# Optimization experiments

Measured on AMD Instinct MI355X. Metric: run time of the kernel, lower is better.

Reference implementation:

```python
import jax, jax.numpy as jnp
import numpy as np
import math

B, S, H, D = 4, 1024, 12, 64   # batch, max_seqlen, heads, head_dim
DIM = H * D                    # 768
L = 512                        # actual per-sequence length (unpadded)
NNZ = B * L                    # total non-pad tokens


def setup_inputs() -> dict:
    key = jax.random.key(0)
    k1, k2, k3 = jax.random.split(key, 3)
    hidden_states = jax.random.normal(k1, (NNZ, DIM), dtype=jnp.float32)
    Wqkv_w = jax.random.normal(k2, (3 * DIM, DIM), dtype=jnp.float32) * 0.02
    Wqkv_b = jnp.zeros((3 * DIM,), dtype=jnp.float32)
    # attn mask: first L tokens of each sequence are real
    attn_mask = (jnp.arange(S)[None, :] < L).astype(jnp.int32) * jnp.ones((B, 1), jnp.int32)
    # additive bias (e.g. ALiBi/relative-pos style) + key-padding penalty
    bias = jax.random.normal(k3, (B, H, S, S), dtype=jnp.float32) * 0.02
    bias = bias + jnp.where(attn_mask[:, None, None, :] == 1, 0.0, -10000.0)
    # flattened positions of non-pad tokens in the padded (B*S,) layout
    indices = (jnp.arange(B)[:, None] * S + jnp.arange(L)[None, :]).reshape(-1).astype(jnp.int64)
    cu_seqlens = (jnp.arange(B + 1) * L).astype(jnp.int32)
    return {
        "hidden_states": hidden_states,
        "Wqkv_w": Wqkv_w,
        "Wqkv_b": Wqkv_b,
        "bias": bias,
        "cu_seqlens": cu_seqlens,
        "max_seqlen_in_batch": S,
        "indices": indices,
        "attn_mask": attn_mask,
    }


def reference(hidden_states, Wqkv_w, Wqkv_b, bias, cu_seqlens, max_seqlen_in_batch, indices, attn_mask):
    b = cu_seqlens.shape[0] - 1
    s = max_seqlen_in_batch
    # QKV projection on unpadded tokens: (nnz, 3*dim)
    qkv = hidden_states @ Wqkv_w.T + Wqkv_b
    # pad_input: scatter tokens into padded (b*s, 3*dim) buffer
    padded = jnp.zeros((b * s, 3 * DIM), dtype=qkv.dtype).at[indices].set(qkv)
    qkv = padded.reshape(b, s, 3, H, D)
    q = qkv[:, :, 0]  # (b, s, h, d)
    k = qkv[:, :, 1]
    v = qkv[:, :, 2]
    scores = jnp.einsum("bqhd,bkhd->bhqk", q, k) / math.sqrt(D) + bias
    probs = jax.nn.softmax(scores, axis=-1)  # dropout p=0 -> identity
    attn = jnp.einsum("bhqk,bkhd->bqhd", probs, v)  # (b, s, h, d)
    # unpad_input_only: gather non-pad rows, flatten heads
    out = attn.reshape(b * s, H * D)[indices]  # (nnz, dim)
    return out
```

## Files before the change

### kernel.cpp

```cpp
#include <hip/hip_runtime.h>
#include <hip/hip_bf16.h>


typedef __attribute__((ext_vector_type(8))) __bf16 bf16x8;
typedef __attribute__((ext_vector_type(4))) __bf16 bf16x4;
typedef __attribute__((ext_vector_type(4))) float  f32x4;

static __device__ __forceinline__ __bf16 tobf(float x) { return (__bf16)x; }

__global__ __launch_bounds__(256) void cvt_bf16(const float* __restrict__ hid,
                                                const float* __restrict__ W,
                                                __bf16* __restrict__ hidB,
                                                __bf16* __restrict__ WB)
{
    int i = blockIdx.x * 256 + threadIdx.x;
    const float* src; __bf16* dst; int off;
    if (i < 196608) { src = hid; dst = hidB; off = i * 8; }
    else            { src = W;   dst = WB;   off = (i - 196608) * 8; }
    float4 a = *reinterpret_cast<const float4*>(src + off);
    float4 b = *reinterpret_cast<const float4*>(src + off + 4);
    bf16x8 o = { tobf(a.x), tobf(a.y), tobf(a.z), tobf(a.w),
                 tobf(b.x), tobf(b.y), tobf(b.z), tobf(b.w) };
    *reinterpret_cast<bf16x8*>(dst + off) = o;
}

__global__ __launch_bounds__(256) void qkv_gemm(
    const __bf16* __restrict__ hidB,
    const __bf16* __restrict__ WB,
    const float*  __restrict__ qb,
    __bf16* __restrict__ Qb, __bf16* __restrict__ Kb, __bf16* __restrict__ Vt)
{
    __shared__ char lds[24 * 1024];

    const int tid = threadIdx.x, lane = tid & 63, wave = tid >> 6;
    const int lo = lane & 15, hi = lane >> 4;
    const int wr = wave >> 1, wc = wave & 1;

    int flat = blockIdx.y * 36 + blockIdx.x;
    flat = (flat & 7) * 72 + (flat >> 3);
    const int f0 = (flat % 36) * 64;
    const int r0 = (flat / 36) * 128;

    const int srow  = tid >> 3;
    const int koffB = (tid & 7) * 16;
    const int kel   = (tid & 7) * 8;

    bf16x8 st[6];
#pragma unroll
    for (int p = 0; p < 4; ++p)
        st[p] = *reinterpret_cast<const bf16x8*>(hidB + (size_t)(r0 + p * 32 + srow) * 768 + kel);
#pragma unroll
    for (int p = 0; p < 2; ++p)
        st[4 + p] = *reinterpret_cast<const bf16x8*>(WB + (size_t)(f0 + p * 32 + srow) * 768 + kel);

    f32x4 acc[4][2] = {};

    for (int kt = 0; kt < 12; ++kt) {
        __syncthreads();
#pragma unroll
        for (int p = 0; p < 4; ++p) {
            int row = p * 32 + srow;
            *reinterpret_cast<bf16x8*>(lds + row * 128 + (koffB ^ ((row & 7) << 4))) = st[p];
        }
#pragma unroll
        for (int p = 0; p < 2; ++p) {
            int row = p * 32 + srow;
            *reinterpret_cast<bf16x8*>(lds + 16384 + row * 128 + (koffB ^ ((row & 7) << 4))) = st[4 + p];
        }
        if (kt < 11) {
            int k0 = (kt + 1) * 64 + kel;
#pragma unroll
            for (int p = 0; p < 4; ++p)
                st[p] = *reinterpret_cast<const bf16x8*>(hidB + (size_t)(r0 + p * 32 + srow) * 768 + k0);
#pragma unroll
            for (int p = 0; p < 2; ++p)
                st[4 + p] = *reinterpret_cast<const bf16x8*>(WB + (size_t)(f0 + p * 32 + srow) * 768 + k0);
        }
        __syncthreads();
#pragma unroll
        for (int ks = 0; ks < 2; ++ks) {
            bf16x8 bfrag[2];
#pragma unroll
            for (int fn = 0; fn < 2; ++fn) {
                int row = wc * 32 + fn * 16 + lo;
                bfrag[fn] = *reinterpret_cast<const bf16x8*>(
                    lds + 16384 + row * 128 + ((ks * 64 + hi * 16) ^ ((row & 7) << 4)));
            }
#pragma unroll
            for (int fm = 0; fm < 4; ++fm) {
                int row = wr * 64 + fm * 16 + lo;
                bf16x8 afrag = *reinterpret_cast<const bf16x8*>(
                    lds + row * 128 + ((ks * 64 + hi * 16) ^ ((row & 7) << 4)));
                acc[fm][0] = __builtin_amdgcn_mfma_f32_16x16x32_bf16(afrag, bfrag[0], acc[fm][0], 0, 0, 0);
                acc[fm][1] = __builtin_amdgcn_mfma_f32_16x16x32_bf16(afrag, bfrag[1], acc[fm][1], 0, 0, 0);
            }
        }
    }

#pragma unroll
    for (int fn = 0; fn < 2; ++fn) {
        int m = f0 + wc * 32 + fn * 16 + lo;
        float bv = qb[m];
        int sel = m / 768;
        int mm  = m - sel * 768;
        int hh  = mm >> 6, d = mm & 63;
        float scale = (sel == 0) ? 0.125f : 1.0f;
#pragma unroll
        for (int fm = 0; fm < 4; ++fm) {
            int t0 = r0 + wr * 64 + fm * 16 + hi * 4;
            int b  = t0 >> 9, q = t0 & 511;
            int bh = b * 12 + hh;
            float v[4];
#pragma unroll
            for (int j = 0; j < 4; ++j) v[j] = (acc[fm][fn][j] + bv) * scale;
            if (sel == 2) {
                bf16x4 pv = { tobf(v[0]), tobf(v[1]), tobf(v[2]), tobf(v[3]) };
                *reinterpret_cast<bf16x4*>(&Vt[((size_t)bh * 64 + d) * 512 + q]) = pv;
            } else {
                __bf16* dst = (sel == 0) ? Qb : Kb;
#pragma unroll
                for (int j = 0; j < 4; ++j)
                    dst[((size_t)bh * 512 + q + j) * 64 + d] = tobf(v[j]);
            }
        }
    }
}

__global__ __launch_bounds__(256) void attn_kernel(
    const __bf16* __restrict__ Qb, const __bf16* __restrict__ Kb,
    const __bf16* __restrict__ Vt, const float* __restrict__ bias,
    float* __restrict__ out)
{
    __shared__ __bf16 P[4][16][40];
    __shared__ float  Obuf[2][16][68];
    __shared__ float  Lbuf[2][16];

    const int tid = threadIdx.x, lane = tid & 63, wave = tid >> 6;
    const int lo = lane & 15, hi = lane >> 4;
    const int qt = wave >> 1, kp = wave & 1;
    const int bh = blockIdx.y, b = bh / 12, hd = bh % 12;
    const int q0 = blockIdx.x * 32 + qt * 16;

    const __bf16* Qp = Qb + ((size_t)bh * 512 + q0) * 64;
    bf16x8 qf0 = *reinterpret_cast<const bf16x8*>(Qp + lo * 64 + hi * 8);
    bf16x8 qf1 = *reinterpret_cast<const bf16x8*>(Qp + lo * 64 + 32 + hi * 8);

    const __bf16* Kbh = Kb + (size_t)bh * 512 * 64;
    const __bf16* Vbh = Vt + (size_t)bh * 64 * 512;
    const float*  bp  = bias + ((size_t)bh * 1024 + q0) * 1024;

    f32x4 oacc[4] = {};
    float lsum[4] = {0.f, 0.f, 0.f, 0.f};
    __bf16* Pw = &P[wave][0][0];

    for (int kc = 0; kc < 8; ++kc) {
        const int k0 = kp * 256 + kc * 32;
        f32x4 c0, c1;
#pragma unroll
        for (int j = 0; j < 4; ++j) {
            const float* r = bp + (size_t)(hi * 4 + j) * 1024 + k0;
            c0[j] = r[lo];
            c1[j] = r[16 + lo];
        }
        const __bf16* kr = Kbh + (size_t)(k0 + lo) * 64 + hi * 8;
        bf16x8 kf00 = *reinterpret_cast<const bf16x8*>(kr);
        bf16x8 kf01 = *reinterpret_cast<const bf16x8*>(kr + 32);
        bf16x8 kf10 = *reinterpret_cast<const bf16x8*>(kr + 16 * 64);
        bf16x8 kf11 = *reinterpret_cast<const bf16x8*>(kr + 16 * 64 + 32);
        f32x4 s0 = __builtin_amdgcn_mfma_f32_16x16x32_bf16(qf0, kf00, c0, 0, 0, 0);
        s0       = __builtin_amdgcn_mfma_f32_16x16x32_bf16(qf1, kf01, s0, 0, 0, 0);
        f32x4 s1 = __builtin_amdgcn_mfma_f32_16x16x32_bf16(qf0, kf10, c1, 0, 0, 0);
        s1       = __builtin_amdgcn_mfma_f32_16x16x32_bf16(qf1, kf11, s1, 0, 0, 0);

#pragma unroll
        for (int j = 0; j < 4; ++j) {
            float p0 = __expf(s0[j]), p1 = __expf(s1[j]);
            lsum[j] += p0 + p1;
            Pw[(hi * 4 + j) * 40 + lo]      = tobf(p0);
            Pw[(hi * 4 + j) * 40 + 16 + lo] = tobf(p1);
        }
        bf16x8 pf = *reinterpret_cast<const bf16x8*>(Pw + lo * 40 + hi * 8);
#pragma unroll
        for (int dt = 0; dt < 4; ++dt) {
            bf16x8 vf = *reinterpret_cast<const bf16x8*>(
                Vbh + (size_t)(dt * 16 + lo) * 512 + k0 + hi * 8);
            oacc[dt] = __builtin_amdgcn_mfma_f32_16x16x32_bf16(pf, vf, oacc[dt], 0, 0, 0);
        }
    }

#pragma unroll
    for (int j = 0; j < 4; ++j) {
        float s = lsum[j];
        s += __shfl_xor(s, 1, 64); s += __shfl_xor(s, 2, 64);
        s += __shfl_xor(s, 4, 64); s += __shfl_xor(s, 8, 64);
        lsum[j] = s;
    }

    if (kp == 1) {
#pragma unroll
        for (int dt = 0; dt < 4; ++dt)
#pragma unroll
            for (int j = 0; j < 4; ++j)
                Obuf[qt][hi * 4 + j][dt * 16 + lo] = oacc[dt][j];
        if (lo == 0) {
#pragma unroll
            for (int j = 0; j < 4; ++j) Lbuf[qt][hi * 4 + j] = lsum[j];
        }
    }
    __syncthreads();
    if (kp == 0) {
#pragma unroll
        for (int j = 0; j < 4; ++j) {
            float inv = 1.0f / (lsum[j] + Lbuf[qt][hi * 4 + j]);
            int q = q0 + hi * 4 + j;
            float* op = out + (size_t)(b * 512 + q) * 768 + hd * 64;
#pragma unroll
            for (int dt = 0; dt < 4; ++dt)
                op[dt * 16 + lo] = (oacc[dt][j] + Obuf[qt][hi * 4 + j][dt * 16 + lo]) * inv;
        }
    }
}

extern "C" void kernel_launch(void* const* d_in, const int* in_sizes, int n_in,
                              void* d_out, int out_size, void* d_ws, size_t ws_size,
                              hipStream_t stream) {
    const float* hid  = (const float*)d_in[0];
    const float* W    = (const float*)d_in[1];
    const float* qb   = (const float*)d_in[2];
    const float* bias = (const float*)d_in[3];
    float* out = (float*)d_out;

    char* ws = (char*)d_ws;
    __bf16* hidB = (__bf16*)(ws);
    __bf16* WB   = (__bf16*)(ws + 3145728);
    __bf16* Qb   = (__bf16*)(ws + 6684672);
    __bf16* Kb   = (__bf16*)(ws + 9830400);
    __bf16* Vt   = (__bf16*)(ws + 12976128);

    cvt_bf16<<<1632, 256, 0, stream>>>(hid, W, hidB, WB);
    qkv_gemm<<<dim3(36, 16), 256, 0, stream>>>(hidB, WB, qb, Qb, Kb, Vt);
    attn_kernel<<<dim3(16, 48), 256, 0, stream>>>(Qb, Kb, Vt, bias, out);
}
```

Before: 297.0 us.

## Fuse fp32-to-bf16 conversion into GEMM, double-buffer LDS, prefetch attention operands

Removes the separate conversion kernel: the QKV GEMM now loads fp32 inputs directly and converts them to bf16 while writing to a double-buffered LDS tile. This cuts one launch and a full round trip of the converted tensors through memory, and replaces two barriers per k-step with one. The attention kernel now prefetches the next chunk's bias, K and V fragments into registers, raises wave priority around the MFMAs, and swizzles the block order across a 1D grid. Together these raise register pressure and double the GEMM's LDS use, which may lower occupancy.

```diff
diff --git a/kernel.cpp b/kernel.cpp
--- a/kernel.cpp
+++ b/kernel.cpp
@@ -8,75 +8,65 @@
 
 static __device__ __forceinline__ __bf16 tobf(float x) { return (__bf16)x; }
 
-__global__ __launch_bounds__(256) void cvt_bf16(const float* __restrict__ hid,
-                                                const float* __restrict__ W,
-                                                __bf16* __restrict__ hidB,
-                                                __bf16* __restrict__ WB)
-{
-    int i = blockIdx.x * 256 + threadIdx.x;
-    const float* src; __bf16* dst; int off;
-    if (i < 196608) { src = hid; dst = hidB; off = i * 8; }
-    else            { src = W;   dst = WB;   off = (i - 196608) * 8; }
-    float4 a = *reinterpret_cast<const float4*>(src + off);
-    float4 b = *reinterpret_cast<const float4*>(src + off + 4);
-    bf16x8 o = { tobf(a.x), tobf(a.y), tobf(a.z), tobf(a.w),
-                 tobf(b.x), tobf(b.y), tobf(b.z), tobf(b.w) };
-    *reinterpret_cast<bf16x8*>(dst + off) = o;
-}
-
 __global__ __launch_bounds__(256) void qkv_gemm(
-    const __bf16* __restrict__ hidB,
-    const __bf16* __restrict__ WB,
-    const float*  __restrict__ qb,
+    const float* __restrict__ hid,
+    const float* __restrict__ W,
+    const float* __restrict__ qb,
     __bf16* __restrict__ Qb, __bf16* __restrict__ Kb, __bf16* __restrict__ Vt)
 {
-    __shared__ char lds[24 * 1024];
+    __shared__ char lds[2][24 * 1024];
 
     const int tid = threadIdx.x, lane = tid & 63, wave = tid >> 6;
     const int lo = lane & 15, hi = lane >> 4;
     const int wr = wave >> 1, wc = wave & 1;
 
-    int flat = blockIdx.y * 36 + blockIdx.x;
+    int flat = blockIdx.x;
     flat = (flat & 7) * 72 + (flat >> 3);
     const int f0 = (flat % 36) * 64;
     const int r0 = (flat / 36) * 128;
 
-    const int srow  = tid >> 3;
-    const int koffB = (tid & 7) * 16;
-    const int kel   = (tid & 7) * 8;
-
-    bf16x8 st[6];
-#pragma unroll
-    for (int p = 0; p < 4; ++p)
-        st[p] = *reinterpret_cast<const bf16x8*>(hidB + (size_t)(r0 + p * 32 + srow) * 768 + kel);
-#pragma unroll
-    for (int p = 0; p < 2; ++p)
-        st[4 + p] = *reinterpret_cast<const bf16x8*>(WB + (size_t)(f0 + p * 32 + srow) * 768 + kel);
+    const int srow = tid >> 3;
+    const int kel  = (tid & 7) * 8;
+
+    const float* abase = hid + (size_t)(r0 + srow) * 768 + kel;
+    const float* bbase = W   + (size_t)(f0 + srow) * 768 + kel;
+
+    float4 sa[6][2];
+    auto LOADT = [&](int kt) {
+        const int k0 = kt * 64;
+#pragma unroll
+        for (int p = 0; p < 4; ++p) {
+            const float* a = abase + (size_t)p * 32 * 768 + k0;
+            sa[p][0] = *reinterpret_cast<const float4*>(a);
+            sa[p][1] = *reinterpret_cast<const float4*>(a + 4);
+        }
+#pragma unroll
+        for (int p = 0; p < 2; ++p) {
+            const float* bsrc = bbase + (size_t)p * 32 * 768 + k0;
+            sa[4 + p][0] = *reinterpret_cast<const float4*>(bsrc);
+            sa[4 + p][1] = *reinterpret_cast<const float4*>(bsrc + 4);
+        }
+    };
+    auto STORET = [&](int buf) {
+#pragma unroll
+        for (int s = 0; s < 6; ++s) {
+            const int row = (s < 4) ? s * 32 + srow : (s - 4) * 32 + srow;
+            const int off = (s < 4) ? 0 : 16384;
+            float4 x = sa[s][0], y = sa[s][1];
+            bf16x8 o = { tobf(x.x), tobf(x.y), tobf(x.z), tobf(x.w),
+                         tobf(y.x), tobf(y.y), tobf(y.z), tobf(y.w) };
+            *reinterpret_cast<bf16x8*>(&lds[buf][off + row * 128 + ((kel * 2) ^ ((row & 7) << 4))]) = o;
+        }
+    };
 
     f32x4 acc[4][2] = {};
-
+    LOADT(0); STORET(0);
+    __syncthreads();
+
+#pragma unroll 1
     for (int kt = 0; kt < 12; ++kt) {
-        __syncthreads();
-#pragma unroll
-        for (int p = 0; p < 4; ++p) {
-            int row = p * 32 + srow;
-            *reinterpret_cast<bf16x8*>(lds + row * 128 + (koffB ^ ((row & 7) << 4))) = st[p];
-        }
-#pragma unroll
-        for (int p = 0; p < 2; ++p) {
-            int row = p * 32 + srow;
-            *reinterpret_cast<bf16x8*>(lds + 16384 + row * 128 + (koffB ^ ((row & 7) << 4))) = st[4 + p];
-        }
-        if (kt < 11) {
-            int k0 = (kt + 1) * 64 + kel;
-#pragma unroll
-            for (int p = 0; p < 4; ++p)
-                st[p] = *reinterpret_cast<const bf16x8*>(hidB + (size_t)(r0 + p * 32 + srow) * 768 + k0);
-#pragma unroll
-            for (int p = 0; p < 2; ++p)
-                st[4 + p] = *reinterpret_cast<const bf16x8*>(WB + (size_t)(f0 + p * 32 + srow) * 768 + k0);
-        }
-        __syncthreads();
+        if (kt < 11) LOADT(kt + 1);
+        const char* L = lds[kt & 1];
 #pragma unroll
         for (int ks = 0; ks < 2; ++ks) {
             bf16x8 bfrag[2];
@@ -84,17 +74,19 @@
             for (int fn = 0; fn < 2; ++fn) {
                 int row = wc * 32 + fn * 16 + lo;
                 bfrag[fn] = *reinterpret_cast<const bf16x8*>(
-                    lds + 16384 + row * 128 + ((ks * 64 + hi * 16) ^ ((row & 7) << 4)));
+                    L + 16384 + row * 128 + ((ks * 64 + hi * 16) ^ ((row & 7) << 4)));
             }
 #pragma unroll
             for (int fm = 0; fm < 4; ++fm) {
                 int row = wr * 64 + fm * 16 + lo;
-                bf16x8 afrag = *reinterpret_cast<const bf16x8*>(
-                    lds + row * 128 + ((ks * 64 + hi * 16) ^ ((row & 7) << 4)));
-                acc[fm][0] = __builtin_amdgcn_mfma_f32_16x16x32_bf16(afrag, bfrag[0], acc[fm][0], 0, 0, 0);
-                acc[fm][1] = __builtin_amdgcn_mfma_f32_16x16x32_bf16(afrag, bfrag[1], acc[fm][1], 0, 0, 0);
+                bf16x8 af = *reinterpret_cast<const bf16x8*>(
+                    L + row * 128 + ((ks * 64 + hi * 16) ^ ((row & 7) << 4)));
+                acc[fm][0] = __builtin_amdgcn_mfma_f32_16x16x32_bf16(af, bfrag[0], acc[fm][0], 0, 0, 0);
+                acc[fm][1] = __builtin_amdgcn_mfma_f32_16x16x32_bf16(af, bfrag[1], acc[fm][1], 0, 0, 0);
             }
         }
+        if (kt < 11) STORET((kt & 1) ^ 1);
+        __syncthreads();
     }
 
 #pragma unroll
@@ -138,8 +130,12 @@
     const int tid = threadIdx.x, lane = tid & 63, wave = tid >> 6;
     const int lo = lane & 15, hi = lane >> 4;
     const int qt = wave >> 1, kp = wave & 1;
-    const int bh = blockIdx.y, b = bh / 12, hd = bh % 12;
-    const int q0 = blockIdx.x * 32 + qt * 16;
+
+    int flat = blockIdx.x;
+    flat = (flat & 7) * 96 + (flat >> 3);
+    const int bh = flat >> 4, qtile = flat & 15;
+    const int b = bh / 12, hd = bh % 12;
+    const int q0 = qtile * 32 + qt * 16;
 
     const __bf16* Qp = Qb + ((size_t)bh * 512 + q0) * 64;
     bf16x8 qf0 = *reinterpret_cast<const bf16x8*>(Qp + lo * 64 + hi * 8);
@@ -149,28 +145,42 @@
     const __bf16* Vbh = Vt + (size_t)bh * 64 * 512;
     const float*  bp  = bias + ((size_t)bh * 1024 + q0) * 1024;
 
+    f32x4 c0[2], c1[2];
+    bf16x8 kf[2][4], vf[2][4];
+    auto LOADC = [&](int kc, int s) {
+        const int k0 = kp * 256 + kc * 32;
+#pragma unroll
+        for (int j = 0; j < 4; ++j) {
+            const float* r = bp + (size_t)(hi * 4 + j) * 1024 + k0;
+            c0[s][j] = r[lo];
+            c1[s][j] = r[16 + lo];
+        }
+        const __bf16* kr = Kbh + (size_t)(k0 + lo) * 64 + hi * 8;
+        kf[s][0] = *reinterpret_cast<const bf16x8*>(kr);
+        kf[s][1] = *reinterpret_cast<const bf16x8*>(kr + 32);
+        kf[s][2] = *reinterpret_cast<const bf16x8*>(kr + 16 * 64);
+        kf[s][3] = *reinterpret_cast<const bf16x8*>(kr + 16 * 64 + 32);
+#pragma unroll
+        for (int dt = 0; dt < 4; ++dt)
+            vf[s][dt] = *reinterpret_cast<const bf16x8*>(
+                Vbh + (size_t)(dt * 16 + lo) * 512 + k0 + hi * 8);
+    };
+
     f32x4 oacc[4] = {};
     float lsum[4] = {0.f, 0.f, 0.f, 0.f};
     __bf16* Pw = &P[wave][0][0];
 
+    LOADC(0, 0);
+#pragma unroll
     for (int kc = 0; kc < 8; ++kc) {
-        const int k0 = kp * 256 + kc * 32;
-        f32x4 c0, c1;
-#pragma unroll
-        for (int j = 0; j < 4; ++j) {
-            const float* r = bp + (size_t)(hi * 4 + j) * 1024 + k0;
-            c0[j] = r[lo];
-            c1[j] = r[16 + lo];
-        }
-        const __bf16* kr = Kbh + (size_t)(k0 + lo) * 64 + hi * 8;
-        bf16x8 kf00 = *reinterpret_cast<const bf16x8*>(kr);
-        bf16x8 kf01 = *reinterpret_cast<const bf16x8*>(kr + 32);
-        bf16x8 kf10 = *reinterpret_cast<const bf16x8*>(kr + 16 * 64);
-        bf16x8 kf11 = *reinterpret_cast<const bf16x8*>(kr + 16 * 64 + 32);
-        f32x4 s0 = __builtin_amdgcn_mfma_f32_16x16x32_bf16(qf0, kf00, c0, 0, 0, 0);
-        s0       = __builtin_amdgcn_mfma_f32_16x16x32_bf16(qf1, kf01, s0, 0, 0, 0);
-        f32x4 s1 = __builtin_amdgcn_mfma_f32_16x16x32_bf16(qf0, kf10, c1, 0, 0, 0);
-        s1       = __builtin_amdgcn_mfma_f32_16x16x32_bf16(qf1, kf11, s1, 0, 0, 0);
+        const int s = kc & 1;
+        if (kc < 7) LOADC(kc + 1, s ^ 1);
+        __builtin_amdgcn_s_setprio(1);
+        f32x4 s0 = __builtin_amdgcn_mfma_f32_16x16x32_bf16(qf0, kf[s][0], c0[s], 0, 0, 0);
+        s0       = __builtin_amdgcn_mfma_f32_16x16x32_bf16(qf1, kf[s][1], s0, 0, 0, 0);
+        f32x4 s1 = __builtin_amdgcn_mfma_f32_16x16x32_bf16(qf0, kf[s][2], c1[s], 0, 0, 0);
+        s1       = __builtin_amdgcn_mfma_f32_16x16x32_bf16(qf1, kf[s][3], s1, 0, 0, 0);
+        __builtin_amdgcn_s_setprio(0);
 
 #pragma unroll
         for (int j = 0; j < 4; ++j) {
@@ -180,12 +190,11 @@
             Pw[(hi * 4 + j) * 40 + 16 + lo] = tobf(p1);
         }
         bf16x8 pf = *reinterpret_cast<const bf16x8*>(Pw + lo * 40 + hi * 8);
-#pragma unroll
-        for (int dt = 0; dt < 4; ++dt) {
-            bf16x8 vf = *reinterpret_cast<const bf16x8*>(
-                Vbh + (size_t)(dt * 16 + lo) * 512 + k0 + hi * 8);
-            oacc[dt] = __builtin_amdgcn_mfma_f32_16x16x32_bf16(pf, vf, oacc[dt], 0, 0, 0);
-        }
+        __builtin_amdgcn_s_setprio(1);
+#pragma unroll
+        for (int dt = 0; dt < 4; ++dt)
+            oacc[dt] = __builtin_amdgcn_mfma_f32_16x16x32_bf16(pf, vf[s][dt], oacc[dt], 0, 0, 0);
+        __builtin_amdgcn_s_setprio(0);
     }
 
 #pragma unroll
@@ -231,13 +240,10 @@
     float* out = (float*)d_out;
 
     char* ws = (char*)d_ws;
-    __bf16* hidB = (__bf16*)(ws);
-    __bf16* WB   = (__bf16*)(ws + 3145728);
-    __bf16* Qb   = (__bf16*)(ws + 6684672);
-    __bf16* Kb   = (__bf16*)(ws + 9830400);
-    __bf16* Vt   = (__bf16*)(ws + 12976128);
-
-    cvt_bf16<<<1632, 256, 0, stream>>>(hid, W, hidB, WB);
-    qkv_gemm<<<dim3(36, 16), 256, 0, stream>>>(hidB, WB, qb, Qb, Kb, Vt);
-    attn_kernel<<<dim3(16, 48), 256, 0, stream>>>(Qb, Kb, Vt, bias, out);
+    __bf16* Qb = (__bf16*)(ws);
+    __bf16* Kb = (__bf16*)(ws + 3145728);
+    __bf16* Vt = (__bf16*)(ws + 6291456);
+
+    qkv_gemm<<<576, 256, 0, stream>>>(hid, W, qb, Qb, Kb, Vt);
+    attn_kernel<<<768, 256, 0, stream>>>(Qb, Kb, Vt, bias, out);
 }
```

Result: no change. 298.5 us (+0.5%).
